# Performance work log

Hardware: AMD Instinct MI355X
Metric: run time of the kernel (lower is better)

Reference implementation:

```python
import jax, jax.numpy as jnp
import numpy as np

C_M, C_Z, H, CH = 256, 128, 8, 32
EPS = 1e-5

def layer_norm(x, g, b):
    mu = jnp.mean(x, axis=-1, keepdims=True)
    var = jnp.mean(jnp.square(x - mu), axis=-1, keepdims=True)
    return (x - mu) * jax.lax.rsqrt(var + EPS) * g + b

def setup_inputs() -> dict:
    key = jax.random.key(0)
    ks = jax.random.split(key, 12)
    B, N, L = 1, 256, 256
    m = jax.random.normal(ks[0], (B, N, L, C_M), dtype=jnp.float32)
    z = jax.random.normal(ks[1], (B, L, L, C_Z), dtype=jnp.float32)
    msa_mask = jax.random.randint(ks[2], (B, N, L), 0, 2, dtype=jnp.int32)
    s = 0.02
    return {
        "m": m, "z": z, "msa_mask": msa_mask,
        "ln_m_g": jnp.ones((C_M,), jnp.float32), "ln_m_b": jnp.zeros((C_M,), jnp.float32),
        "ln_z_g": jnp.ones((C_Z,), jnp.float32), "ln_z_b": jnp.zeros((C_Z,), jnp.float32),
        "Wq": s * jax.random.normal(ks[3], (C_M, H * CH), jnp.float32),
        "Wk": s * jax.random.normal(ks[4], (C_M, H * CH), jnp.float32),
        "Wv": s * jax.random.normal(ks[5], (C_M, H * CH), jnp.float32),
        "Wb": s * jax.random.normal(ks[6], (C_Z, H), jnp.float32),
        "Wg": s * jax.random.normal(ks[7], (C_M, H * CH), jnp.float32),
        "bg": jnp.zeros((H * CH,), jnp.float32),
        "Wo": s * jax.random.normal(ks[8], (H * CH, C_M), jnp.float32),
        "bo": jnp.zeros((C_M,), jnp.float32),
    }

def reference(m, z, msa_mask, ln_m_g, ln_m_b, ln_z_g, ln_z_b,
              Wq, Wk, Wv, Wb, Wg, bg, Wo, bo):
    B, N, L, _ = m.shape
    mn = layer_norm(m, ln_m_g, ln_m_b)          # [B,N,L,c_m]
    zn = layer_norm(z, ln_z_g, ln_z_b)          # [B,L,L,c_z]
    q = (mn @ Wq).reshape(B, N, L, H, CH)
    k = (mn @ Wk).reshape(B, N, L, H, CH)
    v = (mn @ Wv).reshape(B, N, L, H, CH)
    pair_bias = zn @ Wb                          # [B,L,L,H]
    logits = jnp.einsum('bnihc,bnjhc->bnhij', q, k) / np.sqrt(CH).astype(np.float32)
    logits = logits + jnp.transpose(pair_bias, (0, 3, 1, 2))[:, None]  # [B,1,H,i,j]
    # key mask over j: [B,N,1,1,L]
    logits = jnp.where(msa_mask[:, :, None, None, :] == 0, jnp.float32(-1e9), logits)
    attn = jax.nn.softmax(logits, axis=-1)
    out = jnp.einsum('bnhij,bnjhc->bnihc', attn, v)
    gate = jax.nn.sigmoid(mn @ Wg + bg).reshape(B, N, L, H, CH)
    out = (out * gate).reshape(B, N, L, H * CH)
    out = out @ Wo + bo
    out = out * msa_mask[..., None].astype(out.dtype)
    return out
```

## Files before the change

### kernel.cpp

```cpp
#include <hip/hip_runtime.h>

typedef unsigned short ushort_t;
typedef unsigned int uint_t;
typedef __attribute__((ext_vector_type(8))) short bf16x8;
typedef __attribute__((ext_vector_type(4))) float f32x4;

#define EPSV 1e-5f
#define LOG2E 1.4426950408889634f
#define QSC (0.17677669529663687f * LOG2E)

__device__ __forceinline__ float u2f(uint_t x) { return __builtin_bit_cast(float, x); }
__device__ __forceinline__ uint_t f2u(float x) { return __builtin_bit_cast(uint_t, x); }
__device__ __forceinline__ float bflo(uint_t u) { return u2f(u << 16); }
__device__ __forceinline__ float bfhi(uint_t u) { return u2f(u & 0xFFFF0000u); }
__device__ __forceinline__ ushort_t f2bf(float f) {
    uint_t x = f2u(f);
    x += 0x7FFFu + ((x >> 16) & 1u);
    return (ushort_t)(x >> 16);
}
__device__ __forceinline__ uint_t cvtpk(float lo, float hi) {
    uint_t r;
    asm("v_cvt_pk_bf16_f32 %0, %1, %2" : "=v"(r) : "v"(lo), "v"(hi));
    return r;
}
__device__ __forceinline__ float exp2v(float x) {
    float r;
    asm("v_exp_f32 %0, %1" : "=v"(r) : "v"(x));
    return r;
}
__device__ __forceinline__ float rcpv(float x) {
    float r;
    asm("v_rcp_f32 %0, %1" : "=v"(r) : "v"(x));
    return r;
}
__device__ __forceinline__ f32x4 mfma16(bf16x8 a, bf16x8 b, f32x4 c) {
    return __builtin_amdgcn_mfma_f32_16x16x32_bf16(a, b, c, 0, 0, 0);
}
__device__ __forceinline__ float wsum(float v) {
#pragma unroll
    for (int m = 32; m >= 1; m >>= 1) v += __shfl_xor(v, m, 64);
    return v;
}

__global__ __launch_bounds__(256) void k_prep(const float* __restrict__ Wq, const float* __restrict__ Wk,
                                              const float* __restrict__ Wv, const float* __restrict__ Wg,
                                              const float* __restrict__ Wo,
                                              ushort_t* __restrict__ wtT, ushort_t* __restrict__ woT) {
    const int k = blockIdx.x, t = threadIdx.x;
    const int h = t >> 5, c = t & 31;
    wtT[(size_t)(h * 128 +   0 + c) * 256 + k] = f2bf(Wq[k * 256 + t]);
    wtT[(size_t)(h * 128 +  32 + c) * 256 + k] = f2bf(Wk[k * 256 + t]);
    wtT[(size_t)(h * 128 +  64 + c) * 256 + k] = f2bf(Wv[k * 256 + t]);
    wtT[(size_t)(h * 128 +  96 + c) * 256 + k] = f2bf(Wg[k * 256 + t]);
    woT[(size_t)t * 256 + k] = f2bf(Wo[k * 256 + t]);
}

__global__ __launch_bounds__(256) void k_ln_m(const float* __restrict__ m,
                                              const float* __restrict__ g,
                                              const float* __restrict__ b,
                                              ushort_t* __restrict__ mn) {
    const int lane = threadIdx.x & 63;
    const int row  = blockIdx.x * 4 + (threadIdx.x >> 6);
    const float4 x = *(const float4*)(m + (size_t)row * 256 + lane * 4);
    const float mu = wsum(x.x + x.y + x.z + x.w) * (1.f / 256.f);
    const float dx = x.x - mu, dy = x.y - mu, dz = x.z - mu, dw = x.w - mu;
    const float var = wsum(dx * dx + dy * dy + dz * dz + dw * dw) * (1.f / 256.f);
    const float rs = rsqrtf(var + EPSV);
    const float4 gg = *(const float4*)(g + lane * 4);
    const float4 bb = *(const float4*)(b + lane * 4);
    ushort4 o;
    o.x = f2bf(dx * rs * gg.x + bb.x);
    o.y = f2bf(dy * rs * gg.y + bb.y);
    o.z = f2bf(dz * rs * gg.z + bb.z);
    o.w = f2bf(dw * rs * gg.w + bb.w);
    *(ushort4*)(mn + (size_t)row * 256 + lane * 4) = o;
}

__global__ __launch_bounds__(256) void k_pair_bias(const float* __restrict__ z,
                                                   const float* __restrict__ g,
                                                   const float* __restrict__ b,
                                                   const float* __restrict__ Wb,
                                                   float* __restrict__ pb) {
    const int lane = threadIdx.x & 63;
    const int row  = blockIdx.x * 4 + (threadIdx.x >> 6);
    const float2 x = *(const float2*)(z + (size_t)row * 128 + lane * 2);
    const float mu = wsum(x.x + x.y) * (1.f / 128.f);
    const float d0 = x.x - mu, d1 = x.y - mu;
    const float var = wsum(d0 * d0 + d1 * d1) * (1.f / 128.f);
    const float rs = rsqrtf(var + EPSV);
    const float2 gg = *(const float2*)(g + lane * 2);
    const float2 bb = *(const float2*)(b + lane * 2);
    const float z0 = d0 * rs * gg.x + bb.x;
    const float z1 = d1 * rs * gg.y + bb.y;
    const float4 wa0 = *(const float4*)(Wb + lane * 16 + 0);
    const float4 wa1 = *(const float4*)(Wb + lane * 16 + 4);
    const float4 wb0 = *(const float4*)(Wb + lane * 16 + 8);
    const float4 wb1 = *(const float4*)(Wb + lane * 16 + 12);
    float p[8];
    p[0] = z0 * wa0.x + z1 * wb0.x;
    p[1] = z0 * wa0.y + z1 * wb0.y;
    p[2] = z0 * wa0.z + z1 * wb0.z;
    p[3] = z0 * wa0.w + z1 * wb0.w;
    p[4] = z0 * wa1.x + z1 * wb1.x;
    p[5] = z0 * wa1.y + z1 * wb1.y;
    p[6] = z0 * wa1.z + z1 * wb1.z;
    p[7] = z0 * wa1.w + z1 * wb1.w;
#pragma unroll
    for (int h = 0; h < 8; ++h) p[h] = wsum(p[h]);
    float v = p[0];
#pragma unroll
    for (int h = 1; h < 8; ++h) v = (lane == h) ? p[h] : v;
    if (lane < 8) pb[(size_t)lane * 65536 + row] = v * LOG2E;
}

__global__ __launch_bounds__(256, 1) void k_attn(const ushort_t* __restrict__ mn,
                                                 const ushort_t* __restrict__ wtT,
                                                 const float* __restrict__ pb,
                                                 const int* __restrict__ msa_mask,
                                                 const float* __restrict__ bg,
                                                 ushort_t* __restrict__ ao) {
    __shared__ ushort_t k_s[256 * 40];
    __shared__ ushort_t qp_s[256 * 40];
    __shared__ ushort_t vT[32 * 264];
    __shared__ ushort_t gT[32 * 264];
    __shared__ float maskb[256];

    const int t = threadIdx.x;
    const int n = blockIdx.x & 255, h = blockIdx.x >> 8;
    const int w = t >> 6, l = t & 63;
    const int l16 = l & 15, g = l >> 4;

    maskb[t] = msa_mask[n * 256 + t] ? 0.f : -1.5e9f;
    const float bg0 = bg[h * 32 + l16];
    const float bg1 = bg[h * 32 + 16 + l16];

    const ushort_t* mb = mn + (size_t)n * 65536;
    const ushort_t* wb = wtT + (size_t)h * 128 * 256;

#pragma unroll
    for (int chalf = 0; chalf < 2; ++chalf) {
        f32x4 acc[4][4];
#pragma unroll
        for (int rt = 0; rt < 4; ++rt)
#pragma unroll
            for (int ct = 0; ct < 4; ++ct) acc[rt][ct] = (f32x4){0.f, 0.f, 0.f, 0.f};

#pragma unroll
        for (int ks = 0; ks < 8; ++ks) {
            bf16x8 a[4], b[4];
#pragma unroll
            for (int rt = 0; rt < 4; ++rt)
                a[rt] = *(const bf16x8*)(mb + (size_t)(w * 64 + rt * 16 + l16) * 256 + ks * 32 + g * 8);
#pragma unroll
            for (int ct = 0; ct < 4; ++ct)
                b[ct] = *(const bf16x8*)(wb + (size_t)(chalf * 64 + ct * 16 + l16) * 256 + ks * 32 + g * 8);
#pragma unroll
            for (int rt = 0; rt < 4; ++rt)
#pragma unroll
                for (int ct = 0; ct < 4; ++ct)
                    acc[rt][ct] = mfma16(a[rt], b[ct], acc[rt][ct]);
        }
#pragma unroll
        for (int ct = 0; ct < 4; ++ct) {
            const int mat = chalf * 2 + (ct >> 1);
            const int cc = (ct & 1) * 16 + l16;
#pragma unroll
            for (int rt = 0; rt < 4; ++rt) {
                const int i0 = w * 64 + rt * 16 + g * 4;
                const f32x4 v = acc[rt][ct];
                if (mat == 0) {
#pragma unroll
                    for (int r = 0; r < 4; ++r) qp_s[(i0 + r) * 40 + cc] = f2bf(v[r] * QSC);
                } else if (mat == 1) {
#pragma unroll
                    for (int r = 0; r < 4; ++r) k_s[(i0 + r) * 40 + cc] = f2bf(v[r]);
                } else if (mat == 2) {
                    const uint_t lo = cvtpk(v[0], v[1]);
                    const uint_t hi = cvtpk(v[2], v[3]);
                    *(uint2*)(vT + cc * 264 + i0) = make_uint2(lo, hi);
                } else {
                    const float bgc = (ct & 1) ? bg1 : bg0;
                    float gt[4];
#pragma unroll
                    for (int r = 0; r < 4; ++r)
                        gt[r] = rcpv(1.f + exp2v(-(v[r] + bgc) * LOG2E));
                    const uint_t lo = cvtpk(gt[0], gt[1]);
                    const uint_t hi = cvtpk(gt[2], gt[3]);
                    *(uint2*)(gT + cc * 264 + i0) = make_uint2(lo, hi);
                }
            }
        }
    }
    __syncthreads();

    bf16x8 bq[4];
#pragma unroll
    for (int it = 0; it < 4; ++it)
        bq[it] = *(const bf16x8*)&qp_s[(w * 64 + it * 16 + l16) * 40 + g * 8];
    ushort_t* p_w = qp_s + w * 64 * 40;

    const float* pbh = pb + (size_t)h * 65536;
    f32x4 oT[2][4];
#pragma unroll
    for (int ct = 0; ct < 2; ++ct)
#pragma unroll
        for (int it = 0; it < 4; ++it) oT[ct][it] = (f32x4){0.f, 0.f, 0.f, 0.f};
    float lsum[4] = {0.f, 0.f, 0.f, 0.f};

    bf16x8 ak[2], av[2];
    f32x4 pc0[4], pc1[4];
#pragma unroll
    for (int jt = 0; jt < 2; ++jt)
        ak[jt] = *(const bf16x8*)&k_s[(jt * 16 + l16) * 40 + g * 8];
#pragma unroll
    for (int ct = 0; ct < 2; ++ct)
        av[ct] = *(const bf16x8*)&vT[(ct * 16 + l16) * 264 + g * 8];
#pragma unroll
    for (int it = 0; it < 4; ++it) {
        const int i = w * 64 + it * 16 + l16;
        pc0[it] = *(const f32x4*)(pbh + (size_t)i * 256 + g * 4);
        pc1[it] = *(const f32x4*)(pbh + (size_t)i * 256 + 16 + g * 4);
    }

    for (int jc = 0; jc < 8; ++jc) {
        bf16x8 akn[2], avn[2];
        f32x4 pn0[4], pn1[4];
        if (jc < 7) {
            const int j0 = (jc + 1) * 32;
#pragma unroll
            for (int jt = 0; jt < 2; ++jt)
                akn[jt] = *(const bf16x8*)&k_s[(j0 + jt * 16 + l16) * 40 + g * 8];
#pragma unroll
            for (int ct = 0; ct < 2; ++ct)
                avn[ct] = *(const bf16x8*)&vT[(ct * 16 + l16) * 264 + j0 + g * 8];
#pragma unroll
            for (int it = 0; it < 4; ++it) {
                const int i = w * 64 + it * 16 + l16;
                pn0[it] = *(const f32x4*)(pbh + (size_t)i * 256 + j0 + g * 4);
                pn1[it] = *(const f32x4*)(pbh + (size_t)i * 256 + j0 + 16 + g * 4);
            }
        }

        f32x4 st[2][4];
        __builtin_amdgcn_s_setprio(1);
#pragma unroll
        for (int jt = 0; jt < 2; ++jt)
#pragma unroll
            for (int it = 0; it < 4; ++it)
                st[jt][it] = mfma16(ak[jt], bq[it], (f32x4){0.f, 0.f, 0.f, 0.f});
        __builtin_amdgcn_s_setprio(0);

        const f32x4 mk0 = *(const f32x4*)&maskb[jc * 32 + g * 4];
        const f32x4 mk1 = *(const f32x4*)&maskb[jc * 32 + 16 + g * 4];

#pragma unroll
        for (int it = 0; it < 4; ++it) {
            float p0[4], p1[4];
#pragma unroll
            for (int r = 0; r < 4; ++r) {
                p0[r] = exp2v(st[0][it][r] + pc0[it][r] + mk0[r]);
                p1[r] = exp2v(st[1][it][r] + pc1[it][r] + mk1[r]);
            }
#pragma unroll
            for (int r = 0; r < 4; ++r) lsum[it] += p0[r] + p1[r];
            ushort_t* base = p_w + (it * 16 + l16) * 40;
            *(uint2*)(base + g * 4)      = make_uint2(cvtpk(p0[0], p0[1]), cvtpk(p0[2], p0[3]));
            *(uint2*)(base + 16 + g * 4) = make_uint2(cvtpk(p1[0], p1[1]), cvtpk(p1[2], p1[3]));
        }
        __builtin_amdgcn_s_setprio(1);
#pragma unroll
        for (int it = 0; it < 4; ++it) {
            const bf16x8 bp = *(const bf16x8*)&p_w[(it * 16 + l16) * 40 + g * 8];
            oT[0][it] = mfma16(av[0], bp, oT[0][it]);
            oT[1][it] = mfma16(av[1], bp, oT[1][it]);
        }
        __builtin_amdgcn_s_setprio(0);

        if (jc < 7) {
#pragma unroll
            for (int jt = 0; jt < 2; ++jt) ak[jt] = akn[jt];
#pragma unroll
            for (int ct = 0; ct < 2; ++ct) av[ct] = avn[ct];
#pragma unroll
            for (int it = 0; it < 4; ++it) { pc0[it] = pn0[it]; pc1[it] = pn1[it]; }
        }
    }

    float inv[4];
#pragma unroll
    for (int it = 0; it < 4; ++it) {
        float s = lsum[it];
        s += __shfl_xor(s, 16, 64);
        s += __shfl_xor(s, 32, 64);
        inv[it] = rcpv(s);
    }

    __syncthreads();
    ushort_t* oT_s = vT;
#pragma unroll
    for (int ct = 0; ct < 2; ++ct)
#pragma unroll
        for (int it = 0; it < 4; ++it) {
            const int i = w * 64 + it * 16 + l16;
#pragma unroll
            for (int r = 0; r < 4; ++r) {
                const int c = ct * 16 + g * 4 + r;
                const float gate = bflo((uint_t)gT[c * 264 + i]);
                oT_s[c * 264 + i] = f2bf(oT[ct][it][r] * inv[it] * gate);
            }
        }
    __syncthreads();
    ushort_t* aob = ao + (size_t)n * 256 * 256 + h * 32;
#pragma unroll
    for (int iter = 0; iter < 16; ++iter) {
        const int flat = iter * 256 + t;
        const int i = flat >> 4, cp = flat & 15;
        const uint_t lo = oT_s[(2 * cp) * 264 + i];
        const uint_t hi = oT_s[(2 * cp + 1) * 264 + i];
        *(uint_t*)(aob + (size_t)i * 256 + 2 * cp) = lo | (hi << 16);
    }
}

__global__ __launch_bounds__(256, 2) void k_out(const ushort_t* __restrict__ ao,
                                                const ushort_t* __restrict__ woT,
                                                const float* __restrict__ bo,
                                                const int* __restrict__ msa_mask,
                                                float* __restrict__ out) {
    const int t = threadIdx.x;
    const int rb = blockIdx.x * 128;
    const int w = t >> 6, l = t & 63;
    const int l16 = l & 15, g = l >> 4;

#pragma unroll
    for (int ch = 0; ch < 2; ++ch) {
        f32x4 acc[2][8];
#pragma unroll
        for (int rt = 0; rt < 2; ++rt)
#pragma unroll
            for (int ct = 0; ct < 8; ++ct) acc[rt][ct] = (f32x4){0.f, 0.f, 0.f, 0.f};
#pragma unroll
        for (int ks = 0; ks < 8; ++ks) {
            bf16x8 a[2], b[8];
#pragma unroll
            for (int rt = 0; rt < 2; ++rt)
                a[rt] = *(const bf16x8*)(ao + (size_t)(rb + w * 32 + rt * 16 + l16) * 256 + ks * 32 + g * 8);
#pragma unroll
            for (int ct = 0; ct < 8; ++ct)
                b[ct] = *(const bf16x8*)(woT + (size_t)(ch * 128 + ct * 16 + l16) * 256 + ks * 32 + g * 8);
#pragma unroll
            for (int rt = 0; rt < 2; ++rt)
#pragma unroll
                for (int ct = 0; ct < 8; ++ct)
                    acc[rt][ct] = mfma16(a[rt], b[ct], acc[rt][ct]);
        }
#pragma unroll
        for (int rt = 0; rt < 2; ++rt)
#pragma unroll
            for (int ct = 0; ct < 8; ++ct) {
                const int c = ch * 128 + ct * 16 + l16;
                const float boc = bo[c];
#pragma unroll
                for (int r = 0; r < 4; ++r) {
                    const int row = rb + w * 32 + rt * 16 + g * 4 + r;
                    const float mk = msa_mask[row] ? 1.f : 0.f;
                    out[(size_t)row * 256 + c] = (acc[rt][ct][r] + boc) * mk;
                }
            }
    }
}

extern "C" void kernel_launch(void* const* d_in, const int* in_sizes, int n_in,
                              void* d_out, int out_size, void* d_ws, size_t ws_size,
                              hipStream_t stream) {
    const float* m       = (const float*)d_in[0];
    const float* z       = (const float*)d_in[1];
    const int* msa_mask  = (const int*)d_in[2];
    const float* ln_m_g  = (const float*)d_in[3];
    const float* ln_m_b  = (const float*)d_in[4];
    const float* ln_z_g  = (const float*)d_in[5];
    const float* ln_z_b  = (const float*)d_in[6];
    const float* Wq      = (const float*)d_in[7];
    const float* Wk      = (const float*)d_in[8];
    const float* Wv      = (const float*)d_in[9];
    const float* Wb      = (const float*)d_in[10];
    const float* Wg      = (const float*)d_in[11];
    const float* bg      = (const float*)d_in[12];
    const float* Wo      = (const float*)d_in[13];
    const float* bo      = (const float*)d_in[14];
    float* out           = (float*)d_out;

    char* ws = (char*)d_ws;
    ushort_t* mn  = (ushort_t*)(ws);
    float*    pb  = (float*)(ws + 33554432);
    ushort_t* ao  = (ushort_t*)(ws + 35651584);
    ushort_t* wtT = (ushort_t*)(ws + 69206016);
    ushort_t* woT = (ushort_t*)(ws + 69730304);

    k_prep<<<256, 256, 0, stream>>>(Wq, Wk, Wv, Wg, Wo, wtT, woT);
    k_ln_m<<<16384, 256, 0, stream>>>(m, ln_m_g, ln_m_b, mn);
    k_pair_bias<<<16384, 256, 0, stream>>>(z, ln_z_g, ln_z_b, Wb, pb);
    k_attn<<<2048, 256, 0, stream>>>(mn, wtT, pb, msa_mask, bg, ao);
    k_out<<<512, 256, 0, stream>>>(ao, woT, bo, msa_mask, out);
}
```

Baseline: 297.9 us.

## Compute pair bias projection with MFMA and single-pass layernorm statistics

The pair-bias kernel now gives each lane part of a row (16 rows per wave), computes the layernorm mean and variance in one pass with two cross-lane shuffles, and does the 128x8 projection with bf16 MFMA instructions. The weights are pre-packed into a padded MFMA fragment layout in k_prep. This replaces eight full-wave reductions per row and scalar FMAs, cutting shuffle and ALU cost in a memory-bound kernel. In exchange it uses bf16 precision for the projection and E[x^2]-mu^2 variance, which is less numerically robust.

```diff
diff --git a/kernel.cpp b/kernel.cpp
--- a/kernel.cpp
+++ b/kernel.cpp
@@ -44,8 +44,9 @@
 
 __global__ __launch_bounds__(256) void k_prep(const float* __restrict__ Wq, const float* __restrict__ Wk,
                                               const float* __restrict__ Wv, const float* __restrict__ Wg,
-                                              const float* __restrict__ Wo,
-                                              ushort_t* __restrict__ wtT, ushort_t* __restrict__ woT) {
+                                              const float* __restrict__ Wo, const float* __restrict__ Wb,
+                                              ushort_t* __restrict__ wtT, ushort_t* __restrict__ woT,
+                                              ushort_t* __restrict__ wbF) {
     const int k = blockIdx.x, t = threadIdx.x;
     const int h = t >> 5, c = t & 31;
     wtT[(size_t)(h * 128 +   0 + c) * 256 + k] = f2bf(Wq[k * 256 + t]);
@@ -53,6 +54,14 @@
     wtT[(size_t)(h * 128 +  64 + c) * 256 + k] = f2bf(Wv[k * 256 + t]);
     wtT[(size_t)(h * 128 +  96 + c) * 256 + k] = f2bf(Wg[k * 256 + t]);
     woT[(size_t)t * 256 + k] = f2bf(Wo[k * 256 + t]);
+    if (blockIdx.x == 0) {
+        const int ks = t >> 6, lane = t & 63;
+        const int gq = (lane >> 4) & 3, l16w = lane & 15;
+#pragma unroll
+        for (int j = 0; j < 8; ++j)
+            wbF[(ks * 64 + lane) * 8 + j] =
+                (l16w < 8) ? f2bf(Wb[(ks * 32 + gq * 8 + j) * 8 + l16w]) : (ushort_t)0;
+    }
 }
 
 __global__ __launch_bounds__(256) void k_ln_m(const float* __restrict__ m,
@@ -77,40 +86,62 @@
 }
 
 __global__ __launch_bounds__(256) void k_pair_bias(const float* __restrict__ z,
-                                                   const float* __restrict__ g,
-                                                   const float* __restrict__ b,
-                                                   const float* __restrict__ Wb,
+                                                   const float* __restrict__ gam,
+                                                   const float* __restrict__ bet,
+                                                   const ushort_t* __restrict__ wbF,
                                                    float* __restrict__ pb) {
-    const int lane = threadIdx.x & 63;
-    const int row  = blockIdx.x * 4 + (threadIdx.x >> 6);
-    const float2 x = *(const float2*)(z + (size_t)row * 128 + lane * 2);
-    const float mu = wsum(x.x + x.y) * (1.f / 128.f);
-    const float d0 = x.x - mu, d1 = x.y - mu;
-    const float var = wsum(d0 * d0 + d1 * d1) * (1.f / 128.f);
+    const int t = threadIdx.x;
+    const int w = t >> 6, l = t & 63;
+    const int l16 = l & 15, gq = l >> 4;
+    const int row = blockIdx.x * 64 + w * 16 + l16;
+    const float* zr = z + (size_t)row * 128;
+
+    float v[32];
+    float s1 = 0.f, s2 = 0.f;
+#pragma unroll
+    for (int ks = 0; ks < 4; ++ks) {
+        const float4 a0 = *(const float4*)(zr + ks * 32 + gq * 8);
+        const float4 a1 = *(const float4*)(zr + ks * 32 + gq * 8 + 4);
+        v[ks * 8 + 0] = a0.x; v[ks * 8 + 1] = a0.y; v[ks * 8 + 2] = a0.z; v[ks * 8 + 3] = a0.w;
+        v[ks * 8 + 4] = a1.x; v[ks * 8 + 5] = a1.y; v[ks * 8 + 6] = a1.z; v[ks * 8 + 7] = a1.w;
+    }
+#pragma unroll
+    for (int j = 0; j < 32; ++j) { s1 += v[j]; s2 += v[j] * v[j]; }
+    s1 += __shfl_xor(s1, 16, 64); s1 += __shfl_xor(s1, 32, 64);
+    s2 += __shfl_xor(s2, 16, 64); s2 += __shfl_xor(s2, 32, 64);
+    const float mu = s1 * (1.f / 128.f);
+    const float var = s2 * (1.f / 128.f) - mu * mu;
     const float rs = rsqrtf(var + EPSV);
-    const float2 gg = *(const float2*)(g + lane * 2);
-    const float2 bb = *(const float2*)(b + lane * 2);
-    const float z0 = d0 * rs * gg.x + bb.x;
-    const float z1 = d1 * rs * gg.y + bb.y;
-    const float4 wa0 = *(const float4*)(Wb + lane * 16 + 0);
-    const float4 wa1 = *(const float4*)(Wb + lane * 16 + 4);
-    const float4 wb0 = *(const float4*)(Wb + lane * 16 + 8);
-    const float4 wb1 = *(const float4*)(Wb + lane * 16 + 12);
-    float p[8];
-    p[0] = z0 * wa0.x + z1 * wb0.x;
-    p[1] = z0 * wa0.y + z1 * wb0.y;
-    p[2] = z0 * wa0.z + z1 * wb0.z;
-    p[3] = z0 * wa0.w + z1 * wb0.w;
-    p[4] = z0 * wa1.x + z1 * wb1.x;
-    p[5] = z0 * wa1.y + z1 * wb1.y;
-    p[6] = z0 * wa1.z + z1 * wb1.z;
-    p[7] = z0 * wa1.w + z1 * wb1.w;
-#pragma unroll
-    for (int h = 0; h < 8; ++h) p[h] = wsum(p[h]);
-    float v = p[0];
-#pragma unroll
-    for (int h = 1; h < 8; ++h) v = (lane == h) ? p[h] : v;
-    if (lane < 8) pb[(size_t)lane * 65536 + row] = v * LOG2E;
+
+    f32x4 acc = (f32x4){0.f, 0.f, 0.f, 0.f};
+#pragma unroll
+    for (int ks = 0; ks < 4; ++ks) {
+        const float4 g0 = *(const float4*)(gam + ks * 32 + gq * 8);
+        const float4 g1 = *(const float4*)(gam + ks * 32 + gq * 8 + 4);
+        const float4 b0 = *(const float4*)(bet + ks * 32 + gq * 8);
+        const float4 b1 = *(const float4*)(bet + ks * 32 + gq * 8 + 4);
+        const float xn0 = (v[ks * 8 + 0] - mu) * rs * g0.x + b0.x;
+        const float xn1 = (v[ks * 8 + 1] - mu) * rs * g0.y + b0.y;
+        const float xn2 = (v[ks * 8 + 2] - mu) * rs * g0.z + b0.z;
+        const float xn3 = (v[ks * 8 + 3] - mu) * rs * g0.w + b0.w;
+        const float xn4 = (v[ks * 8 + 4] - mu) * rs * g1.x + b1.x;
+        const float xn5 = (v[ks * 8 + 5] - mu) * rs * g1.y + b1.y;
+        const float xn6 = (v[ks * 8 + 6] - mu) * rs * g1.z + b1.z;
+        const float xn7 = (v[ks * 8 + 7] - mu) * rs * g1.w + b1.w;
+        uint4 pk;
+        pk.x = cvtpk(xn0, xn1); pk.y = cvtpk(xn2, xn3);
+        pk.z = cvtpk(xn4, xn5); pk.w = cvtpk(xn6, xn7);
+        const bf16x8 af = __builtin_bit_cast(bf16x8, pk);
+        const bf16x8 bf_ = *(const bf16x8*)(wbF + (ks * 64 + l) * 8);
+        acc = mfma16(af, bf_, acc);
+    }
+    if (l16 < 8) {
+        const int orow = blockIdx.x * 64 + w * 16 + gq * 4;
+        f32x4 o;
+        o[0] = acc[0] * LOG2E; o[1] = acc[1] * LOG2E;
+        o[2] = acc[2] * LOG2E; o[3] = acc[3] * LOG2E;
+        *(f32x4*)(pb + (size_t)l16 * 65536 + orow) = o;
+    }
 }
 
 __global__ __launch_bounds__(256, 1) void k_attn(const ushort_t* __restrict__ mn,
@@ -395,10 +426,11 @@
     ushort_t* ao  = (ushort_t*)(ws + 35651584);
     ushort_t* wtT = (ushort_t*)(ws + 69206016);
     ushort_t* woT = (ushort_t*)(ws + 69730304);
-
-    k_prep<<<256, 256, 0, stream>>>(Wq, Wk, Wv, Wg, Wo, wtT, woT);
+    ushort_t* wbF = (ushort_t*)(ws + 69861376);
+
+    k_prep<<<256, 256, 0, stream>>>(Wq, Wk, Wv, Wg, Wo, Wb, wtT, woT, wbF);
     k_ln_m<<<16384, 256, 0, stream>>>(m, ln_m_g, ln_m_b, mn);
-    k_pair_bias<<<16384, 256, 0, stream>>>(z, ln_z_g, ln_z_b, Wb, pb);
+    k_pair_bias<<<1024, 256, 0, stream>>>(z, ln_z_g, ln_z_b, wbF, pb);
     k_attn<<<2048, 256, 0, stream>>>(mn, wtT, pb, msa_mask, bg, ao);
     k_out<<<512, 256, 0, stream>>>(ao, woT, bo, msa_mask, out);
 }
```

Result: faster. 265.1 us (-11.0%).
